# Kernel optimization log

Measured on AMD Instinct MI355X. Metric: run time of the kernel, lower is better.

Reference implementation:

```python
import jax, jax.numpy as jnp
import numpy as np

N_QUBITS = 8
N_LAYERS = 2


def _apply_1q(state, U, wire, n):
    # state: (bs, 2**n); U: (2,2) fixed or (bs,2,2) batched; wire 0 = most significant
    bs = state.shape[0]
    left = 2 ** wire
    right = 2 ** (n - wire - 1)
    s = state.reshape(bs, left, 2, right)
    if U.ndim == 2:
        s = jnp.einsum('ij,bljr->blir', U, s)
    else:
        s = jnp.einsum('bij,bljr->blir', U, s)
    return s.reshape(bs, -1)


def _apply_ctrl(state, U, control, target, n):
    # apply 2x2 U on `target` where `control` qubit is |1>
    bs = state.shape[0]
    left = 2 ** control
    right = 2 ** (n - control - 1)
    s = state.reshape(bs, left, 2, right)
    s0 = s[:, :, 0, :].reshape(bs, -1)
    s1 = s[:, :, 1, :].reshape(bs, -1)
    t = target if target < control else target - 1  # target index among remaining n-1 wires
    s1 = _apply_1q(s1, U, t, n - 1)
    s = jnp.stack([s0.reshape(bs, left, right), s1.reshape(bs, left, right)], axis=2)
    return s.reshape(bs, -1)


def _rz_batched(theta):
    h = 0.5 * theta
    c, s = jnp.cos(h), jnp.sin(h)
    z = jnp.zeros_like(c)
    row0 = jnp.stack([c - 1j * s, z + 0j], axis=-1)
    row1 = jnp.stack([z + 0j, c + 1j * s], axis=-1)
    return jnp.stack([row0, row1], axis=-2).astype(jnp.complex64)  # (bs,2,2)


def _ry_batched(theta):
    h = 0.5 * theta
    c, s = jnp.cos(h), jnp.sin(h)
    row0 = jnp.stack([c, -s], axis=-1)
    row1 = jnp.stack([s, c], axis=-1)
    return jnp.stack([row0, row1], axis=-2).astype(jnp.complex64)


def _rx_fixed(theta):
    h = 0.5 * theta
    c, s = jnp.cos(h), jnp.sin(h)
    return jnp.stack([jnp.stack([c + 0j, -1j * s]), jnp.stack([-1j * s, c + 0j])]).astype(jnp.complex64)


def _ry_fixed(theta):
    h = 0.5 * theta
    c, s = jnp.cos(h), jnp.sin(h)
    return jnp.stack([jnp.stack([c + 0j, -s + 0j]), jnp.stack([s + 0j, c + 0j])]).astype(jnp.complex64)


def _circuit(X, weights):
    bs, L = X.shape
    n = N_QUBITS
    vpq = L // n + 1  # var_per_qubit
    state = jnp.zeros((bs, 2 ** n), jnp.complex64).at[:, 0].set(1.0)
    H = jnp.asarray(np.array([[1, 1], [1, -1]], np.complex64) / np.sqrt(2))
    # encoding: Hadamard then alternating RZ/RY per qubit
    for q in range(n):
        state = _apply_1q(state, H, q, n)
        for i in range(vpq):
            idx = q * vpq + i
            if idx >= L:
                break
            th = X[:, idx]
            U = _rz_batched(th) if i % 2 == 0 else _ry_batched(th)
            state = _apply_1q(state, U, q, n)
    # entangling ring: layer 0 -> CRX, layer 1 -> CRY ((l+1)%2==0 -> CRY)
    for l in range(N_LAYERS):
        for i in range(n):
            th = weights[l, i]
            U = _ry_fixed(th) if (l + 1) % 2 == 0 else _rx_fixed(th)
            state = _apply_ctrl(state, U, i, (i + 1) % n, n)
    # PauliZ expectation on each wire
    p = state.real ** 2 + state.imag ** 2  # (bs, 256)
    outs = []
    for q in range(n):
        pq = p.reshape(bs, 2 ** q, 2, -1).sum(axis=(1, 3))  # (bs, 2)
        outs.append(pq[:, 0] - pq[:, 1])
    return jnp.stack(outs, axis=1)  # (bs, 8)


def setup_inputs() -> dict:
    key = jax.random.key(0)
    k1, k2 = jax.random.split(key)
    X = jax.random.normal(k1, (16384, 64), dtype=jnp.float32)
    weights = jax.random.normal(k2, (N_LAYERS, N_LAYERS * N_QUBITS), dtype=jnp.float32)
    return {"X": X, "weights": weights}


def reference(X, weights):
    return _circuit(X, weights)
```

## Files before the change

kernel.cpp:

```cpp
#include <hip/hip_runtime.h>

#define DEV __device__ __forceinline__
typedef float f32x2 __attribute__((ext_vector_type(2)));
typedef float f32x4 __attribute__((ext_vector_type(4)));

DEV float shflx(float v, int m) { return __shfl_xor(v, m, 64); }
DEV float rdlane(float v, int l) {
  return __int_as_float(__builtin_amdgcn_readlane(__float_as_int(v), l));
}
DEV f32x2 pkfma(f32x2 a, f32x2 b, f32x2 c) { return __builtin_elementwise_fma(a, b, c); }
DEV f32x2 splat(float x) { return (f32x2){x, x}; }
DEV f32x2 swap2(f32x2 v) { return __builtin_shufflevector(v, v, 1, 0); }
DEV f32x2 cmul(f32x2 P, f32x2 F) {
  f32x2 t = swap2(P);
  f32x2 m = {-t.x, t.y};
  return pkfma(splat(F.y), m, splat(F.x) * P);
}

template <int CTRL>
DEV float dppmov(float v) {
  return __int_as_float(__builtin_amdgcn_update_dpp(
      0, __float_as_int(v), CTRL, 0xf, 0xf, true));
}
template <int M>
DEV float xorl(float v) {
  if constexpr (M == 1)      return dppmov<0xB1>(v);
  else if constexpr (M == 2) return dppmov<0x4E>(v);
  else if constexpr (M == 8) return dppmov<0x128>(v);
  else                       return shflx(v, M);
}

template <int D, bool CRX, int R0, int RS>
DEV void gate_x(f32x2 amp[2][4], int lane, float c1, float s1) {
  const f32x2 C2 = splat(c1);
  if constexpr (CRX) {
    const f32x2 S2 = {s1, -s1};
#pragma unroll
    for (int e = 0; e < 2; ++e)
#pragma unroll
      for (int r = R0; r < 4; r += RS) {
        f32x2 p;
        p.x = xorl<D>(amp[e][r].y);
        p.y = xorl<D>(amp[e][r].x);
        amp[e][r] = pkfma(S2, p, C2 * amp[e][r]);
      }
  } else {
    const float sp = (lane & D) ? s1 : -s1;
    const f32x2 SP = splat(sp);
#pragma unroll
    for (int e = 0; e < 2; ++e)
#pragma unroll
      for (int r = R0; r < 4; r += RS) {
        f32x2 p;
        p.x = xorl<D>(amp[e][r].x);
        p.y = xorl<D>(amp[e][r].y);
        amp[e][r] = pkfma(SP, p, C2 * amp[e][r]);
      }
  }
}

__global__ __launch_bounds__(256, 8) void qsim_kernel(const float* __restrict__ X,
                                                      const float* __restrict__ W,
                                                      float* __restrict__ out, int bs) {
  const int lane = threadIdx.x & 63;
  const int wave = blockIdx.x * (blockDim.x >> 6) + (threadIdx.x >> 6);
  const int b0 = wave * 2;
  if (b0 >= bs) return;

  float w = W[(((lane & 15) >> 3) << 4) + (lane & 7)];
  float sw, cw;
  __sincosf(0.5f * w, &sw, &cw);

  const int ce = (lane >> 3) & 1;
  const int cq = lane & 7;
  int bb = b0 + ce; bb = bb >= bs ? bs - 1 : bb;
  const float* Xrow = X + (size_t)bb * 64;
  float ang[9];
#pragma unroll
  for (int i = 0; i < 9; ++i) {
    int idx = cq * 9 + i;
    idx = idx > 63 ? 63 : idx;
    ang[i] = Xrow[idx];
  }
  const float Hc = 0.70710678118654752440f;
  f32x2 A = {Hc, 0.f}, B = {Hc, 0.f};
#pragma unroll
  for (int i = 0; i < 9; ++i) {
    float s, c;
    __sincosf(0.5f * ang[i], &s, &c);
    if (i > 0) {
      bool dead = (cq == 7);
      c = dead ? 1.f : c;
      s = dead ? 0.f : s;
    }
    if ((i & 1) == 0) {
      f32x2 nA = pkfma((f32x2){s, -s}, swap2(A), splat(c) * A);
      f32x2 nB = pkfma((f32x2){-s, s}, swap2(B), splat(c) * B);
      A = nA; B = nB;
    } else {
      f32x2 nA = pkfma(splat(-s), B, splat(c) * A);
      f32x2 nB = pkfma(splat(c), B, splat(s) * A);
      A = nA; B = nB;
    }
  }

  __shared__ f32x4 ldsAB[4][16];
  const int wvid = (threadIdx.x >> 6) & 3;
  if (lane < 16) ldsAB[wvid][lane] = (f32x4){A.x, A.y, B.x, B.y};
  __builtin_amdgcn_wave_barrier();

  const f32x2* base = (const f32x2*)&ldsAB[wvid][0];
  f32x2 amp[2][4];
#pragma unroll
  for (int e = 0; e < 2; ++e) {
    int bit0 = (lane >> 5) & 1;
    f32x2 P = base[(e * 8 + 0) * 2 + bit0];
#pragma unroll
    for (int q = 1; q <= 5; ++q) {
      int bit = (lane >> (5 - q)) & 1;
      P = cmul(P, base[(e * 8 + q) * 2 + bit]);
    }
    f32x4 F6 = ldsAB[wvid][e * 8 + 6];
    f32x4 F7 = ldsAB[wvid][e * 8 + 7];
    f32x2 A6 = {F6.x, F6.y}, B6 = {F6.z, F6.w};
    f32x2 A7 = {F7.x, F7.y}, B7 = {F7.z, F7.w};
    f32x2 t0 = cmul(P, A6), t1 = cmul(P, B6);
    amp[e][0] = cmul(t0, A7);
    amp[e][1] = cmul(t0, B7);
    amp[e][2] = cmul(t1, A7);
    amp[e][3] = cmul(t1, B7);
  }

#define LANE_GATE(G, CBIT, D)                                         \
  {                                                                   \
    const float cg = rdlane(cw, G), sg = rdlane(sw, G);               \
    const bool act = (lane >> (CBIT)) & 1;                            \
    const float c1 = act ? cg : 1.f, s1 = act ? sg : 0.f;             \
    if (isCRX) gate_x<D, true, 0, 1>(amp, lane, c1, s1);              \
    else       gate_x<D, false, 0, 1>(amp, lane, c1, s1);             \
  }
#pragma unroll
  for (int l = 0; l < 2; ++l) {
    const bool isCRX = (l == 0);
    LANE_GATE(l * 8 + 0, 5, 16)
    LANE_GATE(l * 8 + 1, 4, 8)
    LANE_GATE(l * 8 + 2, 3, 4)
    LANE_GATE(l * 8 + 3, 2, 2)
    LANE_GATE(l * 8 + 4, 1, 1)
    {
      const float cg = rdlane(cw, l * 8 + 5), sg = rdlane(sw, l * 8 + 5);
      const bool act = lane & 1;
      const float c1 = act ? cg : 1.f, s1 = act ? sg : 0.f;
      const f32x2 C2 = splat(c1);
#pragma unroll
      for (int e = 0; e < 2; ++e) {
        f32x2 A0 = amp[e][0], A1 = amp[e][1], A2 = amp[e][2], A3 = amp[e][3];
        if (isCRX) {
          const f32x2 S2 = {s1, -s1};
          amp[e][0] = pkfma(S2, swap2(A2), C2 * A0);
          amp[e][2] = pkfma(S2, swap2(A0), C2 * A2);
          amp[e][1] = pkfma(S2, swap2(A3), C2 * A1);
          amp[e][3] = pkfma(S2, swap2(A1), C2 * A3);
        } else {
          amp[e][0] = pkfma(splat(-s1), A2, C2 * A0);
          amp[e][2] = pkfma(splat(s1), A0, C2 * A2);
          amp[e][1] = pkfma(splat(-s1), A3, C2 * A1);
          amp[e][3] = pkfma(splat(s1), A1, C2 * A3);
        }
      }
    }
    {
      const float cg = rdlane(cw, l * 8 + 6), sg = rdlane(sw, l * 8 + 6);
      const f32x2 C2 = splat(cg);
#pragma unroll
      for (int e = 0; e < 2; ++e) {
        f32x2 A2 = amp[e][2], A3 = amp[e][3];
        if (isCRX) {
          const f32x2 S2 = {sg, -sg};
          amp[e][2] = pkfma(S2, swap2(A3), C2 * A2);
          amp[e][3] = pkfma(S2, swap2(A2), C2 * A3);
        } else {
          amp[e][2] = pkfma(splat(-sg), A3, C2 * A2);
          amp[e][3] = pkfma(splat(sg), A2, C2 * A3);
        }
      }
    }
    {
      const float cg = rdlane(cw, l * 8 + 7), sg = rdlane(sw, l * 8 + 7);
      if (isCRX) gate_x<32, true, 1, 2>(amp, lane, cg, sg);
      else       gate_x<32, false, 1, 2>(amp, lane, cg, sg);
    }
  }
#undef LANE_GATE

  float whtv[2], d6s[2], d7s[2];
#pragma unroll
  for (int e = 0; e < 2; ++e) {
    float p0 = fmaf(amp[e][0].x, amp[e][0].x, amp[e][0].y * amp[e][0].y);
    float p1 = fmaf(amp[e][1].x, amp[e][1].x, amp[e][1].y * amp[e][1].y);
    float p2 = fmaf(amp[e][2].x, amp[e][2].x, amp[e][2].y * amp[e][2].y);
    float p3 = fmaf(amp[e][3].x, amp[e][3].x, amp[e][3].y * amp[e][3].y);
    float t01 = p0 + p1, t23 = p2 + p3;
    float wv = t01 + t23;
    f32x2 D = {t01 - t23,
               (p0 + p2) - (p1 + p3)};
#define STAGE(K, M)                                         \
    {                                                       \
      float pp = xorl<M>(wv);                               \
      wv = pp + (((lane >> K) & 1) ? -wv : wv);             \
      f32x2 pd;                                             \
      pd.x = xorl<M>(D.x);                                  \
      pd.y = xorl<M>(D.y);                                  \
      D = D + pd;                                           \
    }
    STAGE(0, 1) STAGE(1, 2) STAGE(2, 4) STAGE(3, 8) STAGE(4, 16) STAGE(5, 32)
#undef STAGE
    whtv[e] = wv; d6s[e] = D.x; d7s[e] = D.y;
  }

  const int qs = lane & 7;
  const int eid = (lane >> 3) & 1;
  const int src = 32 >> qs;
  float g0 = __shfl(whtv[0], src, 64);
  float g1 = __shfl(whtv[1], src, 64);
  float v0 = (qs == 6) ? d6s[0] : (qs == 7) ? d7s[0] : g0;
  float v1 = (qs == 6) ? d6s[1] : (qs == 7) ? d7s[1] : g1;
  float val = eid ? v1 : v0;
  if (lane < 16 && (b0 + eid) < bs) out[(size_t)b0 * 8 + lane] = val;
}

extern "C" void kernel_launch(void* const* d_in, const int* in_sizes, int n_in,
                              void* d_out, int out_size, void* d_ws, size_t ws_size,
                              hipStream_t stream) {
  const float* X = (const float*)d_in[0];
  const float* W = (const float*)d_in[1];
  float* out = (float*)d_out;
  int bs = in_sizes[0] / 64;
  int waves = (bs + 1) / 2;
  const int waves_per_block = 4;
  const int threads = waves_per_block * 64;
  int blocks = (waves + waves_per_block - 1) / waves_per_block;
  hipLaunchKernelGGL(qsim_kernel, dim3(blocks), dim3(threads), 0, stream, X, W, out, bs);
}
```

Before: 67.08 us.

## Split wave into two 32-lane halves per sample with 8 amplitudes per lane

Changes the state layout so each half-wave holds one batch element, with 5 qubits mapped to lanes and 3 to registers (8 amplitudes per lane), instead of 6 lane qubits and 2 register qubits across two interleaved samples. More gates become in-register pair updates and fewer cross-lane exchanges are needed. The remaining xor-4 and xor-16 exchanges use ds_swizzle in place of generic shuffles. The reduction now has 5 butterfly stages with an extra accumulator, and output selection is per half-wave. Register pressure per lane may rise.

```diff
diff --git a/kernel.cpp b/kernel.cpp
--- a/kernel.cpp
+++ b/kernel.cpp
@@ -4,7 +4,6 @@
 typedef float f32x2 __attribute__((ext_vector_type(2)));
 typedef float f32x4 __attribute__((ext_vector_type(4)));
 
-DEV float shflx(float v, int m) { return __shfl_xor(v, m, 64); }
 DEV float rdlane(float v, int l) {
   return __int_as_float(__builtin_amdgcn_readlane(__float_as_int(v), l));
 }
@@ -24,39 +23,53 @@
 }
 template <int M>
 DEV float xorl(float v) {
-  if constexpr (M == 1)      return dppmov<0xB1>(v);
-  else if constexpr (M == 2) return dppmov<0x4E>(v);
-  else if constexpr (M == 8) return dppmov<0x128>(v);
-  else                       return shflx(v, M);
-}
-
-template <int D, bool CRX, int R0, int RS>
-DEV void gate_x(f32x2 amp[2][4], int lane, float c1, float s1) {
+  if constexpr (M == 1)       return dppmov<0xB1>(v);
+  else if constexpr (M == 2)  return dppmov<0x4E>(v);
+  else if constexpr (M == 8)  return dppmov<0x128>(v);
+  else if constexpr (M == 4)
+    return __int_as_float(__builtin_amdgcn_ds_swizzle(__float_as_int(v), 0x101F));
+  else
+    return __int_as_float(__builtin_amdgcn_ds_swizzle(__float_as_int(v), 0x401F));
+}
+
+template <int M, bool CRX, int R0, int RS>
+DEV void gate_lane(f32x2 amp[8], int lane, float c1, float s1) {
   const f32x2 C2 = splat(c1);
   if constexpr (CRX) {
     const f32x2 S2 = {s1, -s1};
 #pragma unroll
-    for (int e = 0; e < 2; ++e)
-#pragma unroll
-      for (int r = R0; r < 4; r += RS) {
-        f32x2 p;
-        p.x = xorl<D>(amp[e][r].y);
-        p.y = xorl<D>(amp[e][r].x);
-        amp[e][r] = pkfma(S2, p, C2 * amp[e][r]);
-      }
+    for (int r = R0; r < 8; r += RS) {
+      f32x2 p;
+      p.x = xorl<M>(amp[r].y);
+      p.y = xorl<M>(amp[r].x);
+      amp[r] = pkfma(S2, p, C2 * amp[r]);
+    }
   } else {
-    const float sp = (lane & D) ? s1 : -s1;
+    const float sp = (lane & M) ? s1 : -s1;
     const f32x2 SP = splat(sp);
 #pragma unroll
-    for (int e = 0; e < 2; ++e)
-#pragma unroll
-      for (int r = R0; r < 4; r += RS) {
-        f32x2 p;
-        p.x = xorl<D>(amp[e][r].x);
-        p.y = xorl<D>(amp[e][r].y);
-        amp[e][r] = pkfma(SP, p, C2 * amp[e][r]);
-      }
-  }
+    for (int r = R0; r < 8; r += RS) {
+      f32x2 p;
+      p.x = xorl<M>(amp[r].x);
+      p.y = xorl<M>(amp[r].y);
+      amp[r] = pkfma(SP, p, C2 * amp[r]);
+    }
+  }
+}
+
+template <bool CRX>
+DEV void gate_pair(f32x2& aI, f32x2& aJ, float c1, float s1) {
+  const f32x2 C2 = splat(c1);
+  f32x2 nI, nJ;
+  if constexpr (CRX) {
+    const f32x2 S2 = {s1, -s1};
+    nI = pkfma(S2, swap2(aJ), C2 * aI);
+    nJ = pkfma(S2, swap2(aI), C2 * aJ);
+  } else {
+    nI = pkfma(splat(-s1), aJ, C2 * aI);
+    nJ = pkfma(splat(s1), aI, C2 * aJ);
+  }
+  aI = nI; aJ = nJ;
 }
 
 __global__ __launch_bounds__(256, 8) void qsim_kernel(const float* __restrict__ X,
@@ -109,124 +122,106 @@
   if (lane < 16) ldsAB[wvid][lane] = (f32x4){A.x, A.y, B.x, B.y};
   __builtin_amdgcn_wave_barrier();
 
-  const f32x2* base = (const f32x2*)&ldsAB[wvid][0];
-  f32x2 amp[2][4];
-#pragma unroll
-  for (int e = 0; e < 2; ++e) {
-    int bit0 = (lane >> 5) & 1;
-    f32x2 P = base[(e * 8 + 0) * 2 + bit0];
-#pragma unroll
-    for (int q = 1; q <= 5; ++q) {
-      int bit = (lane >> (5 - q)) & 1;
-      P = cmul(P, base[(e * 8 + q) * 2 + bit]);
-    }
-    f32x4 F6 = ldsAB[wvid][e * 8 + 6];
-    f32x4 F7 = ldsAB[wvid][e * 8 + 7];
-    f32x2 A6 = {F6.x, F6.y}, B6 = {F6.z, F6.w};
-    f32x2 A7 = {F7.x, F7.y}, B7 = {F7.z, F7.w};
-    f32x2 t0 = cmul(P, A6), t1 = cmul(P, B6);
-    amp[e][0] = cmul(t0, A7);
-    amp[e][1] = cmul(t0, B7);
-    amp[e][2] = cmul(t1, A7);
-    amp[e][3] = cmul(t1, B7);
-  }
-
-#define LANE_GATE(G, CBIT, D)                                         \
-  {                                                                   \
-    const float cg = rdlane(cw, G), sg = rdlane(sw, G);               \
-    const bool act = (lane >> (CBIT)) & 1;                            \
-    const float c1 = act ? cg : 1.f, s1 = act ? sg : 0.f;             \
-    if (isCRX) gate_x<D, true, 0, 1>(amp, lane, c1, s1);              \
-    else       gate_x<D, false, 0, 1>(amp, lane, c1, s1);             \
-  }
+  const int half = lane >> 5;
+  const int base = half * 8;
+  const f32x2* b2 = (const f32x2*)&ldsAB[wvid][0];
+  f32x2 P = b2[(base + 0) * 2 + ((lane >> 4) & 1)];
+#pragma unroll
+  for (int q = 1; q <= 4; ++q)
+    P = cmul(P, b2[(base + q) * 2 + ((lane >> (4 - q)) & 1)]);
+  f32x4 F5 = ldsAB[wvid][base + 5];
+  f32x4 F6 = ldsAB[wvid][base + 6];
+  f32x4 F7 = ldsAB[wvid][base + 7];
+  f32x2 A5 = {F5.x, F5.y}, B5 = {F5.z, F5.w};
+  f32x2 A6 = {F6.x, F6.y}, B6 = {F6.z, F6.w};
+  f32x2 A7 = {F7.x, F7.y}, B7 = {F7.z, F7.w};
+  f32x2 amp[8];
+  {
+    f32x2 t0 = cmul(P, A5), t1 = cmul(P, B5);
+    f32x2 u00 = cmul(t0, A6), u01 = cmul(t0, B6);
+    f32x2 u10 = cmul(t1, A6), u11 = cmul(t1, B6);
+    amp[0] = cmul(u00, A7); amp[1] = cmul(u00, B7);
+    amp[2] = cmul(u01, A7); amp[3] = cmul(u01, B7);
+    amp[4] = cmul(u10, A7); amp[5] = cmul(u10, B7);
+    amp[6] = cmul(u11, A7); amp[7] = cmul(u11, B7);
+  }
+
 #pragma unroll
   for (int l = 0; l < 2; ++l) {
     const bool isCRX = (l == 0);
-    LANE_GATE(l * 8 + 0, 5, 16)
-    LANE_GATE(l * 8 + 1, 4, 8)
-    LANE_GATE(l * 8 + 2, 3, 4)
-    LANE_GATE(l * 8 + 3, 2, 2)
-    LANE_GATE(l * 8 + 4, 1, 1)
+#define CS(G, CBIT) \
+    const float cg = rdlane(cw, G), sg = rdlane(sw, G); \
+    const bool act = (lane >> (CBIT)) & 1; \
+    const float c1 = act ? cg : 1.f, s1 = act ? sg : 0.f;
+    { CS(l * 8 + 0, 4)
+      if (isCRX) gate_lane<8, true, 0, 1>(amp, lane, c1, s1);
+      else       gate_lane<8, false, 0, 1>(amp, lane, c1, s1); }
+    { CS(l * 8 + 1, 3)
+      if (isCRX) gate_lane<4, true, 0, 1>(amp, lane, c1, s1);
+      else       gate_lane<4, false, 0, 1>(amp, lane, c1, s1); }
+    { CS(l * 8 + 2, 2)
+      if (isCRX) gate_lane<2, true, 0, 1>(amp, lane, c1, s1);
+      else       gate_lane<2, false, 0, 1>(amp, lane, c1, s1); }
+    { CS(l * 8 + 3, 1)
+      if (isCRX) gate_lane<1, true, 0, 1>(amp, lane, c1, s1);
+      else       gate_lane<1, false, 0, 1>(amp, lane, c1, s1); }
+    { CS(l * 8 + 4, 0)
+#pragma unroll
+      for (int r = 0; r < 4; ++r) {
+        if (isCRX) gate_pair<true>(amp[r], amp[r + 4], c1, s1);
+        else       gate_pair<false>(amp[r], amp[r + 4], c1, s1);
+      } }
     {
       const float cg = rdlane(cw, l * 8 + 5), sg = rdlane(sw, l * 8 + 5);
-      const bool act = lane & 1;
-      const float c1 = act ? cg : 1.f, s1 = act ? sg : 0.f;
-      const f32x2 C2 = splat(c1);
-#pragma unroll
-      for (int e = 0; e < 2; ++e) {
-        f32x2 A0 = amp[e][0], A1 = amp[e][1], A2 = amp[e][2], A3 = amp[e][3];
-        if (isCRX) {
-          const f32x2 S2 = {s1, -s1};
-          amp[e][0] = pkfma(S2, swap2(A2), C2 * A0);
-          amp[e][2] = pkfma(S2, swap2(A0), C2 * A2);
-          amp[e][1] = pkfma(S2, swap2(A3), C2 * A1);
-          amp[e][3] = pkfma(S2, swap2(A1), C2 * A3);
-        } else {
-          amp[e][0] = pkfma(splat(-s1), A2, C2 * A0);
-          amp[e][2] = pkfma(splat(s1), A0, C2 * A2);
-          amp[e][1] = pkfma(splat(-s1), A3, C2 * A1);
-          amp[e][3] = pkfma(splat(s1), A1, C2 * A3);
-        }
-      }
+      if (isCRX) { gate_pair<true>(amp[4], amp[6], cg, sg);
+                   gate_pair<true>(amp[5], amp[7], cg, sg); }
+      else       { gate_pair<false>(amp[4], amp[6], cg, sg);
+                   gate_pair<false>(amp[5], amp[7], cg, sg); }
     }
     {
       const float cg = rdlane(cw, l * 8 + 6), sg = rdlane(sw, l * 8 + 6);
-      const f32x2 C2 = splat(cg);
-#pragma unroll
-      for (int e = 0; e < 2; ++e) {
-        f32x2 A2 = amp[e][2], A3 = amp[e][3];
-        if (isCRX) {
-          const f32x2 S2 = {sg, -sg};
-          amp[e][2] = pkfma(S2, swap2(A3), C2 * A2);
-          amp[e][3] = pkfma(S2, swap2(A2), C2 * A3);
-        } else {
-          amp[e][2] = pkfma(splat(-sg), A3, C2 * A2);
-          amp[e][3] = pkfma(splat(sg), A2, C2 * A3);
-        }
-      }
+      if (isCRX) { gate_pair<true>(amp[2], amp[3], cg, sg);
+                   gate_pair<true>(amp[6], amp[7], cg, sg); }
+      else       { gate_pair<false>(amp[2], amp[3], cg, sg);
+                   gate_pair<false>(amp[6], amp[7], cg, sg); }
     }
     {
       const float cg = rdlane(cw, l * 8 + 7), sg = rdlane(sw, l * 8 + 7);
-      if (isCRX) gate_x<32, true, 1, 2>(amp, lane, cg, sg);
-      else       gate_x<32, false, 1, 2>(amp, lane, cg, sg);
-    }
-  }
-#undef LANE_GATE
-
-  float whtv[2], d6s[2], d7s[2];
-#pragma unroll
-  for (int e = 0; e < 2; ++e) {
-    float p0 = fmaf(amp[e][0].x, amp[e][0].x, amp[e][0].y * amp[e][0].y);
-    float p1 = fmaf(amp[e][1].x, amp[e][1].x, amp[e][1].y * amp[e][1].y);
-    float p2 = fmaf(amp[e][2].x, amp[e][2].x, amp[e][2].y * amp[e][2].y);
-    float p3 = fmaf(amp[e][3].x, amp[e][3].x, amp[e][3].y * amp[e][3].y);
-    float t01 = p0 + p1, t23 = p2 + p3;
-    float wv = t01 + t23;
-    f32x2 D = {t01 - t23,
-               (p0 + p2) - (p1 + p3)};
-#define STAGE(K, M)                                         \
-    {                                                       \
-      float pp = xorl<M>(wv);                               \
-      wv = pp + (((lane >> K) & 1) ? -wv : wv);             \
-      f32x2 pd;                                             \
-      pd.x = xorl<M>(D.x);                                  \
-      pd.y = xorl<M>(D.y);                                  \
-      D = D + pd;                                           \
-    }
-    STAGE(0, 1) STAGE(1, 2) STAGE(2, 4) STAGE(3, 8) STAGE(4, 16) STAGE(5, 32)
+      if (isCRX) gate_lane<16, true, 1, 2>(amp, lane, cg, sg);
+      else       gate_lane<16, false, 1, 2>(amp, lane, cg, sg);
+    }
+#undef CS
+  }
+
+  float p[8];
+#pragma unroll
+  for (int r = 0; r < 8; ++r) p[r] = fmaf(amp[r].x, amp[r].x, amp[r].y * amp[r].y);
+  float s01 = p[0] + p[1], s23 = p[2] + p[3], s45 = p[4] + p[5], s67 = p[6] + p[7];
+  float sL = s01 + s23, sH = s45 + s67;
+  float wv = sL + sH;
+  f32x2 D = {sL - sH,
+             (s01 + s45) - (s23 + s67)};
+  float d7 = (p[0] - p[1]) + (p[2] - p[3]) + (p[4] - p[5]) + (p[6] - p[7]);
+
+#define STAGE(K, M)                                   \
+  {                                                   \
+    float pp = xorl<M>(wv);                           \
+    wv = pp + (((lane >> K) & 1) ? -wv : wv);         \
+    f32x2 pd;                                         \
+    pd.x = xorl<M>(D.x);                              \
+    pd.y = xorl<M>(D.y);                              \
+    D = D + pd;                                       \
+    d7 += xorl<M>(d7);                                \
+  }
+  STAGE(0, 1) STAGE(1, 2) STAGE(2, 4) STAGE(3, 8) STAGE(4, 16)
 #undef STAGE
-    whtv[e] = wv; d6s[e] = D.x; d7s[e] = D.y;
-  }
-
-  const int qs = lane & 7;
-  const int eid = (lane >> 3) & 1;
-  const int src = 32 >> qs;
-  float g0 = __shfl(whtv[0], src, 64);
-  float g1 = __shfl(whtv[1], src, 64);
-  float v0 = (qs == 6) ? d6s[0] : (qs == 7) ? d7s[0] : g0;
-  float v1 = (qs == 6) ? d6s[1] : (qs == 7) ? d7s[1] : g1;
-  float val = eid ? v1 : v0;
-  if (lane < 16 && (b0 + eid) < bs) out[(size_t)b0 * 8 + lane] = val;
+
+  const int lpos = lane & 31;
+  const int srcl = (lane & 32) + (16 >> lpos);
+  float g = __shfl(wv, srcl, 64);
+  float val = (lpos == 5) ? D.x : (lpos == 6) ? D.y : (lpos == 7) ? d7 : g;
+  const int brow = b0 + half;
+  if (lpos < 8 && brow < bs) out[(size_t)brow * 8 + lpos] = val;
 }
 
 extern "C" void kernel_launch(void* const* d_in, const int* in_sizes, int n_in,
```

Result: faster. 64.87 us (-3.3%).
